# Performance work log

Measured on AMD Instinct MI355X. Metric: run time of the kernel, lower is better.

The kernel has to match this reference:

```python
import jax, jax.numpy as jnp
from jax import lax
import numpy as np

T, I, H, H2 = 2048, 64, 256, 1024  # time steps, input feats, hidden, hidden2


def _lstm(x, Wih, Whh, bih, bhh):
    """PyTorch-convention LSTM. x: [T, B, I]; Wih: [4H, I]; Whh: [4H, H].
    Gate order i, f, g, o. Returns hidden states [T, B, H]."""
    Hd = Whh.shape[1]
    b = bih + bhh
    xw = jnp.einsum('tbi,gi->tbg', x, Wih) + b  # precompute input projections

    def step(carry, xt):
        h, c = carry
        z = xt + h @ Whh.T
        i, f, g, o = jnp.split(z, 4, axis=-1)
        c = jax.nn.sigmoid(f) * c + jax.nn.sigmoid(i) * jnp.tanh(g)
        h = jax.nn.sigmoid(o) * jnp.tanh(c)
        return (h, c), h

    h0 = jnp.zeros((x.shape[1], Hd), x.dtype)
    _, hs = lax.scan(step, (h0, h0), xw)
    return hs


def setup_inputs() -> dict:
    key = jax.random.key(0)
    ks = jax.random.split(key, 16)
    s1 = 1.0 / np.sqrt(H)
    s2 = 1.0 / np.sqrt(H2)
    d = {
        'x': jax.random.normal(ks[0], (T, I, 21), jnp.float32),
        'Wih1': jax.random.uniform(ks[1], (4 * H, I), jnp.float32, -s1, s1),
        'Whh1': jax.random.uniform(ks[2], (4 * H, H), jnp.float32, -s1, s1),
        'bih1': jax.random.uniform(ks[3], (4 * H,), jnp.float32, -s1, s1),
        'bhh1': jax.random.uniform(ks[4], (4 * H,), jnp.float32, -s1, s1),
        'Wih2': jax.random.uniform(ks[5], (4 * H2, H * 21), jnp.float32, -s2, s2),
        'Whh2': jax.random.uniform(ks[6], (4 * H2, H2), jnp.float32, -s2, s2),
        'bih2': jax.random.uniform(ks[7], (4 * H2,), jnp.float32, -s2, s2),
        'bhh2': jax.random.uniform(ks[8], (4 * H2,), jnp.float32, -s2, s2),
        'Wih3': jax.random.uniform(ks[9], (4 * H, H2), jnp.float32, -s1, s1),
        'Whh3': jax.random.uniform(ks[10], (4 * H, H), jnp.float32, -s1, s1),
        'bih3': jax.random.uniform(ks[11], (4 * H,), jnp.float32, -s1, s1),
        'bhh3': jax.random.uniform(ks[12], (4 * H,), jnp.float32, -s1, s1),
        'Wfc': jax.random.uniform(ks[13], (21, H), jnp.float32, -s1, s1),
        'bfc': jax.random.uniform(ks[14], (21,), jnp.float32, -s1, s1),
    }
    return d


def reference(x, Wih1, Whh1, bih1, bhh1, Wih2, Whh2, bih2, bhh2,
              Wih3, Whh3, bih3, bhh3, Wfc, bfc):
    # The 21-iteration torch loop runs lstm1 independently on each of the 21
    # channel slices with batch=1; fold the 21 channels into the batch dim.
    x1 = jnp.transpose(x, (0, 2, 1))           # [T, 21, I]
    h1 = _lstm(x1, Wih1, Whh1, bih1, bhh1)     # [T, 21, H]
    # x_torch[:, :, i*H:(i+1)*H] = channel i -> channel-major concat
    xcat = h1.reshape(T, 1, 21 * H)            # [T, 1, 21H]
    h2 = _lstm(xcat, Wih2, Whh2, bih2, bhh2)   # [T, 1, H2]
    h3 = _lstm(h2, Wih3, Whh3, bih3, bhh3)     # [T, 1, H]
    out = h3 @ Wfc.T + bfc                     # [T, 1, 21]
    return out
```

## Files before the change

### kernel.cpp

```cpp
#include <hip/hip_runtime.h>


#define T_STEPS 2048
#define SENT 0xFFFFFFFFu

using f4v   = __attribute__((ext_vector_type(4))) float;
using s8v   = __attribute__((ext_vector_type(8))) short;
using u16x8 = __attribute__((ext_vector_type(8))) unsigned short;
using u32x4 = __attribute__((ext_vector_type(4))) unsigned;

__device__ __forceinline__ unsigned short f2bf(float v) {
  unsigned u = __float_as_uint(v);
  u = (u + 0x7FFFu + ((u >> 16) & 1u)) >> 16;
  return (unsigned short)u;
}
__device__ __forceinline__ float bf2f(unsigned short b) {
  return __uint_as_float(((unsigned)b) << 16);
}
__device__ __forceinline__ unsigned packhl(float v) {
  unsigned short hb = f2bf(v);
  unsigned short lb = f2bf(v - bf2f(hb));
  return (((unsigned)hb) << 16) | lb;
}
__device__ __forceinline__ float unpackhl(unsigned p) {
  return __uint_as_float(p & 0xFFFF0000u) + __uint_as_float(p << 16);
}
__device__ __forceinline__ float sigm(float x) { return 1.0f / (1.0f + __expf(-x)); }
__device__ __forceinline__ float tanh_f(float x) {
  float ax = fabsf(x);
  float e = __expf(-2.0f * ax);
  float t = (1.0f - e) / (1.0f + e);
  return copysignf(t, x);
}
__device__ __forceinline__ unsigned ld_agent32(const unsigned* p) {
  return __hip_atomic_load(p, __ATOMIC_RELAXED, __HIP_MEMORY_SCOPE_AGENT);
}
__device__ __forceinline__ void st_agent32(unsigned* p, unsigned v) {
  __hip_atomic_store(p, v, __ATOMIC_RELAXED, __HIP_MEMORY_SCOPE_AGENT);
}
__device__ __forceinline__ void ctr_add(unsigned* p) {
  __hip_atomic_fetch_add(p, 1u, __ATOMIC_RELAXED, __HIP_MEMORY_SCOPE_AGENT);
}
__device__ __forceinline__ void poll_ctr(const unsigned* p, unsigned tgt) {
  unsigned n = 0;
  while (ld_agent32(p) < tgt) {
    if (++n > (1u << 22)) break;
    __builtin_amdgcn_s_sleep(4);
  }
}
__device__ __forceinline__ u32x4 ld16_coh(const unsigned* addr) {
  u32x4 c;
  asm volatile("global_load_dwordx4 %0, %1, off sc0 sc1\n\t"
               "s_waitcnt vmcnt(0)"
               : "=&v"(c) : "v"(addr) : "memory");
  return c;
}
#define VMCNT0() asm volatile("s_waitcnt vmcnt(0)" ::: "memory")

#define ISSUE4(r0, r1, r2, r3, ad)                                          \
  asm volatile(                                                             \
      "global_load_dwordx4 %0, %4, off sc0 sc1\n\t"                         \
      "global_load_dwordx4 %1, %4, off offset:1024 sc0 sc1\n\t"             \
      "global_load_dwordx4 %2, %4, off offset:2048 sc0 sc1\n\t"             \
      "global_load_dwordx4 %3, %4, off offset:3072 sc0 sc1"                 \
      : "=&v"(r0), "=&v"(r1), "=&v"(r2), "=&v"(r3) : "v"(ad) : "memory")
#define OK4(r0, r1, r2, r3)                                                 \
  ((r0[0] != SENT) && (r0[1] != SENT) && (r0[2] != SENT) && (r0[3] != SENT) && \
   (r1[0] != SENT) && (r1[1] != SENT) && (r1[2] != SENT) && (r1[3] != SENT) && \
   (r2[0] != SENT) && (r2[1] != SENT) && (r2[2] != SENT) && (r2[3] != SENT) && \
   (r3[0] != SENT) && (r3[1] != SENT) && (r3[2] != SENT) && (r3[3] != SENT))

#define L16(M) M(0) M(1) M(2) M(3) M(4) M(5) M(6) M(7) M(8) M(9) M(10) M(11) \
  M(12) M(13) M(14) M(15)
#define L32(M) L16(M) M(16) M(17) M(18) M(19) M(20) M(21) M(22) M(23) M(24) \
  M(25) M(26) M(27) M(28) M(29) M(30) M(31)
#define L64(M) L32(M) M(32) M(33) M(34) M(35) M(36) \
  M(37) M(38) M(39) M(40) M(41) M(42) M(43) M(44) M(45) M(46) M(47) M(48) \
  M(49) M(50) M(51) M(52) M(53) M(54) M(55) M(56) M(57) M(58) M(59) M(60) \
  M(61) M(62) M(63)

__device__ __forceinline__ void unpack8(u32x4 a, u32x4 b, u16x8& hi, u16x8& lo) {
#pragma unroll
  for (int j = 0; j < 4; ++j) {
    hi[j]     = (unsigned short)(a[j] >> 16);
    lo[j]     = (unsigned short)(a[j] & 0xFFFFu);
    hi[4 + j] = (unsigned short)(b[j] >> 16);
    lo[4 + j] = (unsigned short)(b[j] & 0xFFFFu);
  }
}

__device__ void gemm_tile_packed64(
    const unsigned* __restrict__ Ap, const unsigned short* __restrict__ Bh,
    const unsigned short* __restrict__ Bl, const float* __restrict__ b1,
    const float* __restrict__ b2, unsigned* __restrict__ C,
    int tm, int tn, int K, int N, char* smem)
{
  unsigned short* lds = (unsigned short*)smem;
  const size_t m0 = (size_t)tm * 64, n0 = (size_t)tn * 128;
  const int tid = threadIdx.x, lane = tid & 63, w = tid >> 6;
  const int wr = w >> 1, wc = w & 1;
  const int srow = tid >> 2, sc8 = (tid & 3) * 8;

  const unsigned* pA = Ap + m0 * K;
  const unsigned short* pBh = Bh + n0 * K;
  const unsigned short* pBl = Bl + n0 * K;

  f4v acc[2][4];
#pragma unroll
  for (int i = 0; i < 2; ++i)
#pragma unroll
    for (int j = 0; j < 4; ++j) acc[i][j] = f4v{0.f, 0.f, 0.f, 0.f};

  u32x4 a00, a01;
  u16x8 s4, s5, s6, s7;
#define LOADK(k0)                                                           \
  a00 = *(const u32x4*)(pA + (size_t)srow * K + (k0) + sc8);                \
  a01 = *(const u32x4*)(pA + (size_t)srow * K + (k0) + sc8 + 4);            \
  s4 = *(const u16x8*)(pBh + (size_t)srow * K + (k0) + sc8);                \
  s5 = *(const u16x8*)(pBh + (size_t)(srow + 64) * K + (k0) + sc8);         \
  s6 = *(const u16x8*)(pBl + (size_t)srow * K + (k0) + sc8);                \
  s7 = *(const u16x8*)(pBl + (size_t)(srow + 64) * K + (k0) + sc8);

  LOADK(0);
  const int fr = lane & 15, fko = (lane >> 4) * 8;
  for (int k0 = 0; k0 < K; k0 += 32) {
    u16x8 h0, l0;
    unpack8(a00, a01, h0, l0);
    *(u16x8*)&lds[0     + srow * 32 + sc8] = h0;
    *(u16x8*)&lds[2048  + srow * 32 + sc8] = l0;
    *(u16x8*)&lds[4096  +  srow       * 32 + sc8] = s4;
    *(u16x8*)&lds[4096  + (srow + 64) * 32 + sc8] = s5;
    *(u16x8*)&lds[8192  +  srow       * 32 + sc8] = s6;
    *(u16x8*)&lds[8192  + (srow + 64) * 32 + sc8] = s7;
    __syncthreads();
    if (k0 + 32 < K) { LOADK(k0 + 32); }
    s8v afh[2], afl[2], bfh[4], bfl[4];
#pragma unroll
    for (int i = 0; i < 2; ++i) {
      int ar = (32 * wr + 16 * i + fr) * 32 + fko;
      afh[i] = *(const s8v*)&lds[0 + ar];
      afl[i] = *(const s8v*)&lds[2048 + ar];
    }
#pragma unroll
    for (int i = 0; i < 4; ++i) {
      int br = (64 * wc + 16 * i + fr) * 32 + fko;
      bfh[i] = *(const s8v*)&lds[4096 + br];
      bfl[i] = *(const s8v*)&lds[8192 + br];
    }
#pragma unroll
    for (int mi = 0; mi < 2; ++mi)
#pragma unroll
      for (int ni = 0; ni < 4; ++ni) {
        acc[mi][ni] = __builtin_amdgcn_mfma_f32_16x16x32_bf16(afh[mi], bfh[ni], acc[mi][ni], 0, 0, 0);
        acc[mi][ni] = __builtin_amdgcn_mfma_f32_16x16x32_bf16(afh[mi], bfl[ni], acc[mi][ni], 0, 0, 0);
        acc[mi][ni] = __builtin_amdgcn_mfma_f32_16x16x32_bf16(afl[mi], bfh[ni], acc[mi][ni], 0, 0, 0);
      }
    __syncthreads();
  }
#undef LOADK
  const int er = (lane >> 4) * 4, ec = lane & 15;
#pragma unroll
  for (int ni = 0; ni < 4; ++ni) {
    size_t col = n0 + 64 * wc + 16 * ni + ec;
    float bv = b1[col] + b2[col];
#pragma unroll
    for (int mi = 0; mi < 2; ++mi) {
      size_t row = m0 + 32 * wr + 16 * mi + er;
#pragma unroll
      for (int rr = 0; rr < 4; ++rr)
        st_agent32(&C[(row + rr) * N + col], __float_as_uint(acc[mi][ni][rr] + bv));
    }
  }
}

__global__ __launch_bounds__(256, 1) void mega_kernel(
    const float* __restrict__ x,
    const float* __restrict__ Wih1, const float* __restrict__ Whh1,
    const float* __restrict__ bih1, const float* __restrict__ bhh1,
    const float* __restrict__ Whh2,
    const float* __restrict__ bih2, const float* __restrict__ bhh2,
    const float* __restrict__ Whh3,
    const float* __restrict__ bih3, const float* __restrict__ bhh3,
    unsigned* __restrict__ h1r0, unsigned* __restrict__ h2r0,
    unsigned* __restrict__ h3r0, unsigned* __restrict__ cnt,
    unsigned* __restrict__ h1rows, unsigned* __restrict__ h2rows,
    unsigned* __restrict__ h3rows,
    float* __restrict__ xw2, float* __restrict__ xw3,
    const unsigned short* __restrict__ wih2h, const unsigned short* __restrict__ wih2l,
    const unsigned short* __restrict__ wih3h, const unsigned short* __restrict__ wih3l)
{
  __shared__ __align__(16) char smem[24576];
  unsigned* ready1 = cnt + 0;
  unsigned* done2  = cnt + 32;
  unsigned* ready2 = cnt + 64;
  unsigned* done3  = cnt + 96;
  const int wg = blockIdx.x;
  const int widx = threadIdx.x >> 6, lane = threadIdx.x & 63;

  if (wg < 84) {
    const int c = wg / 4, sub = wg % 4;
    const int gwv = sub * 4 + widx;
    const int u16i = lane & 15, g = lane >> 4;
    const int grow = g * 256 + gwv * 16 + u16i;

    const f4v* wsrc = (const f4v*)(Whh1 + (size_t)grow * 256);
    const f4v* xsrc = (const f4v*)(Wih1 + (size_t)grow * 64);
#define DH(i) f4v m##i = wsrc[i];
#define DX(i) f4v n##i = xsrc[i];
    L64(DH)
    L16(DX)
#undef DH
#undef DX
    const float bias = bih1[grow] + bhh1[grow];

    float* const hbuf = (float*)smem;
    float cst = 0.0f;
    float xpre = (widx == 0) ? x[(size_t)lane * 21 + c] : 0.0f;

    for (int t = 0; t < T_STEPS; ++t) {
      float* const hb = hbuf + (t & 1) * 320;
      if (widx == 0) {
        hb[256 + lane] = xpre;
        if (t + 1 < T_STEPS) xpre = x[(size_t)(t + 1) * 1344 + lane * 21 + c];
        const unsigned* src = t ? h1rows + (size_t)(t - 1) * 5376 + c * 256
                                : h1r0 + c * 256;
        const unsigned* addr = src + 4 * lane;
        u32x4 c0;
        unsigned n = 0;
        for (;;) {
          c0 = ld16_coh(addr);
          bool ok = (c0[0] != SENT) && (c0[1] != SENT) &&
                    (c0[2] != SENT) && (c0[3] != SENT);
          if (ok || ++n > (1u << 18)) break;
          __builtin_amdgcn_s_sleep(1);
        }
        *(f4v*)&hb[4 * lane] = f4v{unpackhl(c0[0]), unpackhl(c0[1]),
                                   unpackhl(c0[2]), unpackhl(c0[3])};
      }
      __syncthreads();
      __builtin_amdgcn_s_setprio(1);
      float a0 = 0, a1 = 0, a2 = 0, a3 = 0;
#define FH(i) { f4v h4 = *(const f4v*)&hb[4 * i]; \
  a0 = fmaf(m##i[0], h4[0], a0); a1 = fmaf(m##i[1], h4[1], a1); \
  a2 = fmaf(m##i[2], h4[2], a2); a3 = fmaf(m##i[3], h4[3], a3); }
#define FX(i) { f4v x4 = *(const f4v*)&hb[256 + 4 * i]; \
  a0 = fmaf(n##i[0], x4[0], a0); a1 = fmaf(n##i[1], x4[1], a1); \
  a2 = fmaf(n##i[2], x4[2], a2); a3 = fmaf(n##i[3], x4[3], a3); }
      L64(FH)
      L16(FX)
#undef FH
#undef FX
      float z = (a0 + a1) + (a2 + a3) + bias;
      float zi = __shfl(z, u16i);
      float zf = __shfl(z, 16 + u16i);
      float zg = __shfl(z, 32 + u16i);
      float zo = __shfl(z, 48 + u16i);
      if (lane < 16) {
        float cn = sigm(zf) * cst + sigm(zi) * tanh_f(zg);
        float hn = sigm(zo) * tanh_f(cn);
        cst = cn;
        st_agent32(&h1rows[(size_t)t * 5376 + c * 256 + gwv * 16 + lane], packhl(hn));
      }
      __builtin_amdgcn_s_setprio(0);
      if ((t & 63) == 63) {
        VMCNT0();
        if (lane == 0) ctr_add(&ready1[t >> 6]);
      }
    }
  } else if (wg < 212) {
    const int gw = (wg - 84) * 4 + widx;
    const int r8 = lane >> 3, e = lane & 7;
    const int g = r8 >> 1, u = r8 & 1;
    const int grow = g * 1024 + 2 * gw + u;

    const f4v* wsrc = (const f4v*)(Whh2 + (size_t)grow * 1024 + e * 128);
#define DW(i) f4v w##i = wsrc[i];
    L32(DW)
#undef DW
    asm volatile("" : "+v"(w0), "+v"(w1), "+v"(w2), "+v"(w3),
                      "+v"(w4), "+v"(w5), "+v"(w6), "+v"(w7));
    asm volatile("" : "+v"(w8), "+v"(w9), "+v"(w10), "+v"(w11),
                      "+v"(w12), "+v"(w13), "+v"(w14), "+v"(w15));
    asm volatile("" : "+v"(w16), "+v"(w17), "+v"(w18), "+v"(w19),
                      "+v"(w20), "+v"(w21), "+v"(w22), "+v"(w23));
    asm volatile("" : "+v"(w24), "+v"(w25), "+v"(w26), "+v"(w27),
                      "+v"(w28), "+v"(w29), "+v"(w30), "+v"(w31));

    float* const hbuf = (float*)smem;
    const int sb = (lane >> 5) * 132 + 4 * (lane & 31);
    const int ug = lane & 1;

    float cst = 0.0f;
    float xwi = 0, xwf = 0, xwg = 0, xwo = 0;

    for (int t = 0; t < T_STEPS; ++t) {
      if ((t & 63) == 0) {
        poll_ctr(&done2[t >> 6], 32);
        if (lane < 2) {
          const float* xp = xw2 + (size_t)t * 4096 + 2 * gw + lane;
          xwi = xp[0]; xwf = xp[1024]; xwg = xp[2048]; xwo = xp[3072];
        }
      }
      float* const hls = hbuf + (t & 1) * 1056;
      if (widx == 0) {
        const unsigned* src = t ? h2rows + (size_t)(t - 1) * 1024 : h2r0;
        const unsigned* addr = src + 4 * lane;
        u32x4 c0, c1, c2, c3;
        unsigned n = 0;
        for (;;) {
          ISSUE4(c0, c1, c2, c3, addr);
          asm volatile("s_waitcnt vmcnt(0)"
                       : "+v"(c0), "+v"(c1), "+v"(c2), "+v"(c3) :: "memory");
          if (OK4(c0, c1, c2, c3) || ++n > (1u << 18)) break;
          __builtin_amdgcn_s_sleep(1);
        }
        *(f4v*)&hls[sb]       = f4v{unpackhl(c0[0]), unpackhl(c0[1]), unpackhl(c0[2]), unpackhl(c0[3])};
        *(f4v*)&hls[sb + 264] = f4v{unpackhl(c1[0]), unpackhl(c1[1]), unpackhl(c1[2]), unpackhl(c1[3])};
        *(f4v*)&hls[sb + 528] = f4v{unpackhl(c2[0]), unpackhl(c2[1]), unpackhl(c2[2]), unpackhl(c2[3])};
        *(f4v*)&hls[sb + 792] = f4v{unpackhl(c3[0]), unpackhl(c3[1]), unpackhl(c3[2]), unpackhl(c3[3])};
      }
      __syncthreads();
      __builtin_amdgcn_s_setprio(1);
      const float* const eb = hls + e * 132;
      float a0 = 0, a1 = 0, a2 = 0, a3 = 0;
#define FW(i) { f4v h4 = *(const f4v*)&eb[4 * i]; \
  a0 = fmaf(w##i[0], h4[0], a0); a1 = fmaf(w##i[1], h4[1], a1); \
  a2 = fmaf(w##i[2], h4[2], a2); a3 = fmaf(w##i[3], h4[3], a3); }
      L32(FW)
#undef FW
      float z = (a0 + a1) + (a2 + a3);
      z += __shfl_xor(z, 1);
      z += __shfl_xor(z, 2);
      z += __shfl_xor(z, 4);
      float zi = __shfl(z, (0 + ug) * 8);
      float zf = __shfl(z, (2 + ug) * 8);
      float zg2 = __shfl(z, (4 + ug) * 8);
      float zo = __shfl(z, (6 + ug) * 8);
      if (lane < 2) {
        float vi = zi + xwi, vf = zf + xwf, vg = zg2 + xwg, vo = zo + xwo;
        float cn = sigm(vf) * cst + sigm(vi) * tanh_f(vg);
        float hn = sigm(vo) * tanh_f(cn);
        cst = cn;
        st_agent32(&h2rows[(size_t)t * 1024 + 2 * gw + lane], packhl(hn));
      }
      __builtin_amdgcn_s_setprio(0);
      if ((t & 63) == 63) {
        VMCNT0();
        if (lane == 0) ctr_add(&ready2[t >> 6]);
      }
      if (lane < 2 && t + 1 < T_STEPS && ((t + 1) & 63) != 0) {
        const float* xp = xw2 + (size_t)(t + 1) * 4096 + 2 * gw + lane;
        xwi = xp[0]; xwf = xp[1024]; xwg = xp[2048]; xwo = xp[3072];
      }
    }
  } else if (wg < 216) {
    const int gw = (wg - 212) * 4 + widx;
    const int u16i = lane & 15, g = lane >> 4;
    const int grow = g * 256 + gw * 16 + u16i;

    const f4v* wsrc = (const f4v*)(Whh3 + (size_t)grow * 256);
#define DW(i) f4v w##i = wsrc[i];
    L64(DW)
#undef DW

    float* const hbuf = (float*)smem;
    float cst = 0.0f;
    float xwn = 0.0f;

    for (int t = 0; t < T_STEPS; ++t) {
      float xwv;
      if ((t & 63) == 0) {
        poll_ctr(&done3[t >> 6], 8);
        xwv = xw3[(size_t)t * 1024 + grow];
      } else xwv = xwn;
      float* const hb = hbuf + (t & 1) * 256;
      if (widx == 0) {
        const unsigned* src = t ? h3rows + (size_t)(t - 1) * 256 : h3r0;
        const unsigned* addr = src + 4 * lane;
        u32x4 c0;
        unsigned n = 0;
        for (;;) {
          c0 = ld16_coh(addr);
          bool ok = (c0[0] != SENT) && (c0[1] != SENT) &&
                    (c0[2] != SENT) && (c0[3] != SENT);
          if (ok || ++n > (1u << 18)) break;
          __builtin_amdgcn_s_sleep(1);
        }
        *(f4v*)&hb[4 * lane] = f4v{__uint_as_float(c0[0]), __uint_as_float(c0[1]),
                                   __uint_as_float(c0[2]), __uint_as_float(c0[3])};
      }
      __syncthreads();
      __builtin_amdgcn_s_setprio(1);
      float a0 = 0, a1 = 0, a2 = 0, a3 = 0;
#define FW(i) { f4v h4 = *(const f4v*)&hb[4 * i]; \
  a0 = fmaf(w##i[0], h4[0], a0); a1 = fmaf(w##i[1], h4[1], a1); \
  a2 = fmaf(w##i[2], h4[2], a2); a3 = fmaf(w##i[3], h4[3], a3); }
      L64(FW)
#undef FW
      float z = (a0 + a1) + (a2 + a3) + xwv;
      float zi = __shfl(z, u16i);
      float zf = __shfl(z, 16 + u16i);
      float zg = __shfl(z, 32 + u16i);
      float zo = __shfl(z, 48 + u16i);
      if (lane < 16) {
        float cn = sigm(zf) * cst + sigm(zi) * tanh_f(zg);
        float hn = sigm(zo) * tanh_f(cn);
        cst = cn;
        st_agent32(&h3rows[(size_t)t * 256 + gw * 16 + lane], __float_as_uint(hn));
      }
      __builtin_amdgcn_s_setprio(0);
      if (t + 1 < T_STEPS && ((t + 1) & 63) != 0)
        xwn = xw3[(size_t)(t + 1) * 1024 + grow];
    }
  } else if (wg < 244) {
    const int pw = wg - 216;
    for (int i = pw; i < 1024; i += 28) {
      int tm = i >> 5, tn = i & 31;
      poll_ctr(&ready1[tm], 336);
      gemm_tile_packed64(h1rows, wih2h, wih2l, bih2, bhh2,
                         (unsigned*)xw2, tm, tn, 5376, 4096, smem);
      VMCNT0();
      __syncthreads();
      if (threadIdx.x == 0) ctr_add(&done2[tm]);
      __syncthreads();
    }
  } else {
    const int pw = wg - 244;
    for (int i = pw; i < 256; i += 8) {
      int tm = i >> 3, tn = i & 7;
      poll_ctr(&ready2[tm], 512);
      gemm_tile_packed64(h2rows, wih3h, wih3l, bih3, bhh3,
                         (unsigned*)xw3, tm, tn, 1024, 1024, smem);
      VMCNT0();
      __syncthreads();
      if (threadIdx.x == 0) ctr_add(&done3[tm]);
      __syncthreads();
    }
  }
}

__global__ void split_kernel(const float* __restrict__ src,
                             unsigned short* __restrict__ hi,
                             unsigned short* __restrict__ lo, int n) {
  int i = blockIdx.x * 256 + threadIdx.x;
  if (i < n) {
    float v = src[i];
    unsigned short hb = f2bf(v);
    hi[i] = hb;
    lo[i] = f2bf(v - bf2f(hb));
  }
}

__global__ void fc_kernel(const float* __restrict__ h3, const float* __restrict__ Wfc,
                          const float* __restrict__ bfc, float* __restrict__ out) {
  int t = blockIdx.x, m = threadIdx.x;
  if (m < 21) {
    const float* hp = h3 + (size_t)t * 256;
    const float* wp = Wfc + m * 256;
    float a = 0.0f;
#pragma unroll 8
    for (int j = 0; j < 256; ++j) a = fmaf(wp[j], hp[j], a);
    out[t * 21 + m] = a + bfc[m];
  }
}

extern "C" void kernel_launch(void* const* d_in, const int* in_sizes, int n_in,
                              void* d_out, int out_size, void* d_ws, size_t ws_size,
                              hipStream_t stream) {
  const float* x    = (const float*)d_in[0];
  const float* Wih1 = (const float*)d_in[1];
  const float* Whh1 = (const float*)d_in[2];
  const float* bih1 = (const float*)d_in[3];
  const float* bhh1 = (const float*)d_in[4];
  const float* Wih2 = (const float*)d_in[5];
  const float* Whh2 = (const float*)d_in[6];
  const float* bih2 = (const float*)d_in[7];
  const float* bhh2 = (const float*)d_in[8];
  const float* Wih3 = (const float*)d_in[9];
  const float* Whh3 = (const float*)d_in[10];
  const float* bih3 = (const float*)d_in[11];
  const float* bhh3 = (const float*)d_in[12];
  const float* Wfc  = (const float*)d_in[13];
  const float* bfc  = (const float*)d_in[14];
  float* out = (float*)d_out;

  const size_t WS_NEEDED = 188776448;
  if (ws_size < WS_NEEDED) return;
  char* ws = (char*)d_ws;
  unsigned* h1r0 = (unsigned*)(ws + 0);
  unsigned* h2r0 = (unsigned*)(ws + 21504);
  unsigned* h3r0 = (unsigned*)(ws + 25600);
  unsigned* cnt  = (unsigned*)(ws + 26624);
  unsigned* h1rows = (unsigned*)(ws + 32768);
  unsigned* h2rows = (unsigned*)(ws + 44072960);
  unsigned* h3rows = (unsigned*)(ws + 52461568);
  float* xw2 = (float*)(ws + 54558720);
  float* xw3 = (float*)(ws + 88113152);
  unsigned short* wih2h = (unsigned short*)(ws + 96501760);
  unsigned short* wih2l = (unsigned short*)(ws + 140541952);
  unsigned short* wih3h = (unsigned short*)(ws + 184582144);
  unsigned short* wih3l = (unsigned short*)(ws + 186679296);

  hipMemsetAsync(ws, 0, 32768, stream);
  hipMemsetAsync(ws + 32768, 0xFF, 54525952, stream);

  const int nW2 = 4096 * 5376;
  split_kernel<<<(nW2 + 255) / 256, 256, 0, stream>>>(Wih2, wih2h, wih2l, nW2);
  const int nW3 = 1024 * 1024;
  split_kernel<<<(nW3 + 255) / 256, 256, 0, stream>>>(Wih3, wih3h, wih3l, nW3);

  mega_kernel<<<252, 256, 0, stream>>>(
      x, Wih1, Whh1, bih1, bhh1,
      Whh2, bih2, bhh2, Whh3, bih3, bhh3,
      h1r0, h2r0, h3r0, cnt,
      h1rows, h2rows, h3rows, xw2, xw3,
      wih2h, wih2l, wih3h, wih3l);

  fc_kernel<<<2048, 64, 0, stream>>>((const float*)h3rows, Wfc, bfc, out);
}
```

Before: 9.030 ms.

## Relay layer-2 hidden state through per-XCD hub buffers to cut polling traffic

Layer-2 workgroups no longer all spin on the global h2rows row. Eight hub workgroups, one per class (wg&7, likely one per XCD), poll it and republish the values as 64-bit words tagged with the step index into a double-buffered per-class hub buffer. The other workgroups poll that hub and accept a value when its tag matches, with a periodic fallback read of the original row. The aim is to cut contention and cross-die coherent traffic on the critical per-step exchange, at the cost of an extra relay hop, more load instructions, and relying on 64-bit stores being atomic.

```diff
diff --git a/kernel.cpp b/kernel.cpp
--- a/kernel.cpp
+++ b/kernel.cpp
@@ -8,6 +8,8 @@
 using s8v   = __attribute__((ext_vector_type(8))) short;
 using u16x8 = __attribute__((ext_vector_type(8))) unsigned short;
 using u32x4 = __attribute__((ext_vector_type(4))) unsigned;
+
+union HU { unsigned long long u; unsigned v[2]; float f[2]; };
 
 __device__ __forceinline__ unsigned short f2bf(float v) {
   unsigned u = __float_as_uint(v);
@@ -69,6 +71,12 @@
    (r1[0] != SENT) && (r1[1] != SENT) && (r1[2] != SENT) && (r1[3] != SENT) && \
    (r2[0] != SENT) && (r2[1] != SENT) && (r2[2] != SENT) && (r2[3] != SENT) && \
    (r3[0] != SENT) && (r3[1] != SENT) && (r3[2] != SENT) && (r3[3] != SENT))
+#define OKQ(r) ((r[0] != SENT) && (r[1] != SENT) && (r[2] != SENT) && (r[3] != SENT))
+
+#define HUBLD(lo, hi, ad)                                                   \
+  asm volatile("global_load_dwordx4 %0, %2, off sc0\n\t"                    \
+               "global_load_dwordx4 %1, %2, off offset:16 sc0"              \
+               : "=&v"(lo), "=&v"(hi) : "v"(ad) : "memory")
 
 #define L16(M) M(0) M(1) M(2) M(3) M(4) M(5) M(6) M(7) M(8) M(9) M(10) M(11) \
   M(12) M(13) M(14) M(15)
@@ -185,6 +193,7 @@
     unsigned* __restrict__ h3r0, unsigned* __restrict__ cnt,
     unsigned* __restrict__ h1rows, unsigned* __restrict__ h2rows,
     unsigned* __restrict__ h3rows,
+    unsigned long long* __restrict__ hubbuf,
     float* __restrict__ xw2, float* __restrict__ xw3,
     const unsigned short* __restrict__ wih2h, const unsigned short* __restrict__ wih2l,
     const unsigned short* __restrict__ wih3h, const unsigned short* __restrict__ wih3l)
@@ -272,6 +281,9 @@
     const int r8 = lane >> 3, e = lane & 7;
     const int g = r8 >> 1, u = r8 & 1;
     const int grow = g * 1024 + 2 * gw + u;
+    const int cls = wg & 7;
+    const bool is_hub = (wg - 84) < 8;
+    unsigned long long* const hubb = hubbuf + (size_t)cls * 2048;
 
     const f4v* wsrc = (const f4v*)(Whh2 + (size_t)grow * 1024 + e * 128);
 #define DW(i) f4v w##i = wsrc[i];
@@ -303,21 +315,77 @@
       }
       float* const hls = hbuf + (t & 1) * 1056;
       if (widx == 0) {
-        const unsigned* src = t ? h2rows + (size_t)(t - 1) * 1024 : h2r0;
-        const unsigned* addr = src + 4 * lane;
-        u32x4 c0, c1, c2, c3;
-        unsigned n = 0;
-        for (;;) {
-          ISSUE4(c0, c1, c2, c3, addr);
+        u32x4 q0 = {0,0,0,0}, q1 = {0,0,0,0}, q2 = {0,0,0,0}, q3 = {0,0,0,0};
+        if (t == 0) {
+          ISSUE4(q0, q1, q2, q3, h2r0 + 4 * lane);
           asm volatile("s_waitcnt vmcnt(0)"
-                       : "+v"(c0), "+v"(c1), "+v"(c2), "+v"(c3) :: "memory");
-          if (OK4(c0, c1, c2, c3) || ++n > (1u << 18)) break;
-          __builtin_amdgcn_s_sleep(1);
+                       : "+v"(q0), "+v"(q1), "+v"(q2), "+v"(q3) :: "memory");
+        } else if (is_hub) {
+          const unsigned* addr = h2rows + (size_t)(t - 1) * 1024 + 4 * lane;
+          unsigned n = 0;
+          for (;;) {
+            ISSUE4(q0, q1, q2, q3, addr);
+            asm volatile("s_waitcnt vmcnt(0)"
+                         : "+v"(q0), "+v"(q1), "+v"(q2), "+v"(q3) :: "memory");
+            if (OK4(q0, q1, q2, q3) || ++n > (1u << 18)) break;
+            __builtin_amdgcn_s_sleep(1);
+          }
+          unsigned long long* hp = hubb + (size_t)(t & 1) * 1024 + 4 * lane;
+          const unsigned tt = (unsigned)t;
+#pragma unroll
+          for (int j = 0; j < 4; ++j) {
+            HU a; a.v[0] = q0[j]; a.v[1] = tt; hp[j]       = a.u;
+            HU b; b.v[0] = q1[j]; b.v[1] = tt; hp[256 + j] = b.u;
+            HU c; c.v[0] = q2[j]; c.v[1] = tt; hp[512 + j] = c.u;
+            HU d; d.v[0] = q3[j]; d.v[1] = tt; hp[768 + j] = d.u;
+          }
+        } else {
+          const unsigned long long* hp = hubb + (size_t)(t & 1) * 1024 + 4 * lane;
+          const unsigned* daddr = h2rows + (size_t)(t - 1) * 1024 + 4 * lane;
+          const unsigned tt = (unsigned)t;
+          bool d0 = false, d1 = false, d2 = false, d3 = false;
+          u32x4 lo0 = {0,0,0,0}, hi0 = {0,0,0,0}, lo1 = {0,0,0,0}, hi1 = {0,0,0,0};
+          u32x4 lo2 = {0,0,0,0}, hi2 = {0,0,0,0}, lo3 = {0,0,0,0}, hi3 = {0,0,0,0};
+          unsigned n = 0;
+          for (;;) {
+            if (!d0) HUBLD(lo0, hi0, hp);
+            if (!d1) HUBLD(lo1, hi1, hp + 256);
+            if (!d2) HUBLD(lo2, hi2, hp + 512);
+            if (!d3) HUBLD(lo3, hi3, hp + 768);
+            asm volatile("s_waitcnt vmcnt(0)"
+                         : "+v"(lo0), "+v"(hi0), "+v"(lo1), "+v"(hi1),
+                           "+v"(lo2), "+v"(hi2), "+v"(lo3), "+v"(hi3) :: "memory");
+            if (!d0 && lo0[1] == tt && lo0[3] == tt && hi0[1] == tt && hi0[3] == tt) {
+              q0 = u32x4{lo0[0], lo0[2], hi0[0], hi0[2]}; d0 = true;
+            }
+            if (!d1 && lo1[1] == tt && lo1[3] == tt && hi1[1] == tt && hi1[3] == tt) {
+              q1 = u32x4{lo1[0], lo1[2], hi1[0], hi1[2]}; d1 = true;
+            }
+            if (!d2 && lo2[1] == tt && lo2[3] == tt && hi2[1] == tt && hi2[3] == tt) {
+              q2 = u32x4{lo2[0], lo2[2], hi2[0], hi2[2]}; d2 = true;
+            }
+            if (!d3 && lo3[1] == tt && lo3[3] == tt && hi3[1] == tt && hi3[3] == tt) {
+              q3 = u32x4{lo3[0], lo3[2], hi3[0], hi3[2]}; d3 = true;
+            }
+            if ((d0 && d1 && d2 && d3) || n > (1u << 18)) break;
+            if ((++n & 7) == 7) {
+              u32x4 f0, f1, f2, f3;
+              ISSUE4(f0, f1, f2, f3, daddr);
+              asm volatile("s_waitcnt vmcnt(0)"
+                           : "+v"(f0), "+v"(f1), "+v"(f2), "+v"(f3) :: "memory");
+              if (!d0 && OKQ(f0)) { q0 = f0; d0 = true; }
+              if (!d1 && OKQ(f1)) { q1 = f1; d1 = true; }
+              if (!d2 && OKQ(f2)) { q2 = f2; d2 = true; }
+              if (!d3 && OKQ(f3)) { q3 = f3; d3 = true; }
+              if (d0 && d1 && d2 && d3) break;
+            }
+            __builtin_amdgcn_s_sleep(1);
+          }
         }
-        *(f4v*)&hls[sb]       = f4v{unpackhl(c0[0]), unpackhl(c0[1]), unpackhl(c0[2]), unpackhl(c0[3])};
-        *(f4v*)&hls[sb + 264] = f4v{unpackhl(c1[0]), unpackhl(c1[1]), unpackhl(c1[2]), unpackhl(c1[3])};
-        *(f4v*)&hls[sb + 528] = f4v{unpackhl(c2[0]), unpackhl(c2[1]), unpackhl(c2[2]), unpackhl(c2[3])};
-        *(f4v*)&hls[sb + 792] = f4v{unpackhl(c3[0]), unpackhl(c3[1]), unpackhl(c3[2]), unpackhl(c3[3])};
+        *(f4v*)&hls[sb]       = f4v{unpackhl(q0[0]), unpackhl(q0[1]), unpackhl(q0[2]), unpackhl(q0[3])};
+        *(f4v*)&hls[sb + 264] = f4v{unpackhl(q1[0]), unpackhl(q1[1]), unpackhl(q1[2]), unpackhl(q1[3])};
+        *(f4v*)&hls[sb + 528] = f4v{unpackhl(q2[0]), unpackhl(q2[1]), unpackhl(q2[2]), unpackhl(q2[3])};
+        *(f4v*)&hls[sb + 792] = f4v{unpackhl(q3[0]), unpackhl(q3[1]), unpackhl(q3[2]), unpackhl(q3[3])};
       }
       __syncthreads();
       __builtin_amdgcn_s_setprio(1);
@@ -484,7 +552,7 @@
   const float* bfc  = (const float*)d_in[14];
   float* out = (float*)d_out;
 
-  const size_t WS_NEEDED = 188776448;
+  const size_t WS_NEEDED = 188907520;
   if (ws_size < WS_NEEDED) return;
   char* ws = (char*)d_ws;
   unsigned* h1r0 = (unsigned*)(ws + 0);
@@ -500,9 +568,11 @@
   unsigned short* wih2l = (unsigned short*)(ws + 140541952);
   unsigned short* wih3h = (unsigned short*)(ws + 184582144);
   unsigned short* wih3l = (unsigned short*)(ws + 186679296);
+  unsigned long long* hubbuf = (unsigned long long*)(ws + 188776448);
 
   hipMemsetAsync(ws, 0, 32768, stream);
   hipMemsetAsync(ws + 32768, 0xFF, 54525952, stream);
+  hipMemsetAsync(ws + 188776448, 0xFF, 131072, stream);
 
   const int nW2 = 4096 * 5376;
   split_kernel<<<(nW2 + 255) / 256, 256, 0, stream>>>(Wih2, wih2h, wih2l, nW2);
@@ -513,7 +583,7 @@
       x, Wih1, Whh1, bih1, bhh1,
       Whh2, bih2, bhh2, Whh3, bih3, bhh3,
       h1r0, h2r0, h3r0, cnt,
-      h1rows, h2rows, h3rows, xw2, xw3,
+      h1rows, h2rows, h3rows, hubbuf, xw2, xw3,
       wih2h, wih2l, wih3h, wih3l);
 
   fc_kernel<<<2048, 64, 0, stream>>>((const float*)h3rows, Wfc, bfc, out);
```

After: 12.59 ms. 1.39x slower.
